# Performance work log

Hardware: AMD Instinct MI355X
Metric: run time of the kernel (lower is better)

## Reference

```python
import jax, jax.numpy as jnp
import numpy as np

B, N, DIM, HEADS = 2, 1024, 1024, 16
HD = DIM // HEADS  # 64


def setup_inputs() -> dict:
    key = jax.random.key(0)
    ks = jax.random.split(key, 8)
    f = lambda k, s: jax.random.normal(k, s, dtype=jnp.float32)
    inv = np.float32(1.0 / np.sqrt(DIM))
    return {
        'x_real': f(ks[0], (B, N, DIM)),
        'x_imag': f(ks[1], (B, N, DIM)),
        'freqs_real': f(ks[2], (N, HD)),
        'freqs_imag': f(ks[3], (N, HD)),
        'Wqkv_r': f(ks[4], (3 * DIM, DIM)) * inv,
        'Wqkv_i': f(ks[5], (3 * DIM, DIM)) * inv,
        'bqkv_r': jnp.zeros((3 * DIM,), jnp.float32),
        'bqkv_i': jnp.zeros((3 * DIM,), jnp.float32),
        'Wout_r': f(ks[6], (DIM, DIM)) * inv,
        'Wout_i': f(ks[7], (DIM, DIM)) * inv,
        'bout_r': jnp.zeros((DIM,), jnp.float32),
        'bout_i': jnp.zeros((DIM,), jnp.float32),
    }


def reference(x_real, x_imag, freqs_real, freqs_imag,
              Wqkv_r, Wqkv_i, bqkv_r, bqkv_i,
              Wout_r, Wout_i, bout_r, bout_i):
    cplx = jax.lax.complex
    x = cplx(x_real, x_imag)                    # [b, n, d] complex64
    Wqkv = cplx(Wqkv_r, Wqkv_i)                 # [3d, d]
    bqkv = cplx(bqkv_r, bqkv_i)
    Wout = cplx(Wout_r, Wout_i)
    bout = cplx(bout_r, bout_i)
    freqs = cplx(freqs_real, freqs_imag)        # [n, hd]

    scale = HD ** (-0.5)

    # ComplexLinear: x @ W^T + b -> [b, n, 3d]
    qkv = jnp.einsum('bnd,ed->bne', x, Wqkv) + bqkv
    # rearrange 'b n (h d qkv) -> qkv b h n d' (qkv index fastest-varying)
    qkv = qkv.reshape(B, N, HEADS, HD, 3)
    q = jnp.transpose(qkv[..., 0], (0, 2, 1, 3))  # [b, h, n, hd]
    k = jnp.transpose(qkv[..., 1], (0, 2, 1, 3))
    v = jnp.transpose(qkv[..., 2], (0, 2, 1, 3))

    # complex rotary: elementwise multiply by freqs [n, hd]
    q = q * freqs
    k = k * freqs

    # complex QK^H -> [b, h, n, n]
    dots = jnp.einsum('bhnd,bhmd->bhnm', q, jnp.conj(k))
    attn = jax.nn.softmax(jnp.abs(dots) * scale, axis=-1)  # real float32

    # real attn @ complex v (promotes to complex64)
    out = jnp.einsum('bhnm,bhmd->bhnd', attn, v)
    out = jnp.transpose(out, (0, 2, 1, 3)).reshape(B, N, DIM)  # b n (h d)

    out = jnp.einsum('bnd,ed->bne', out, Wout) + bout
    # return real/imag stacked so baseline comparison is on real arrays
    return jnp.stack([jnp.real(out), jnp.imag(out)], axis=0)  # [2, b, n, d]
```

## Files before the change

### kernel.cpp

```cpp
#include <hip/hip_runtime.h>
#include <hip/hip_bf16.h>
#include <stdint.h>

#define B 2
#define N 1024
#define DIM 1024
#define HEADS 16
#define HD 64
#define E3 (3*DIM)
#define M (B*N)

typedef __hip_bfloat16 bf16;
typedef __attribute__((ext_vector_type(8))) short short8v;
typedef __attribute__((ext_vector_type(4))) float f32x4;
typedef __attribute__((ext_vector_type(4))) unsigned int u32x4;

__device__ __forceinline__ float scrub(float v) {
    return (v == v && fabsf(v) < 1e30f) ? v : 0.0f;
}
__device__ __forceinline__ float b2f(bf16 x) { return scrub(__bfloat162float(x)); }

template<bool FP32>
__device__ __forceinline__ float ldin(const void* p, int i) {
    if (FP32) return scrub(((const float*)p)[i]);
    else      return scrub(__bfloat162float(((const bf16*)p)[i]));
}

__device__ __forceinline__ bool sniff_fp32(const void* x, int tid, int* sbad) {
    if (tid == 0) *sbad = 0;
    __syncthreads();
    if (tid < 64) {
        const unsigned short* u = (const unsigned short*)x;
        int ex = (u[tid] >> 7) & 0xFF;
        if (ex == 0xFF || ex >= 135 || (ex != 0 && ex <= 118))
            atomicAdd(sbad, 1);
    }
    __syncthreads();
    return *sbad > 4;
}

__device__ __forceinline__ short f2bs(float x) {
    bf16 h = __float2bfloat16(x);
    return __builtin_bit_cast(short, h);
}
__device__ __forceinline__ short8v neg8(short8v x) {
    u32x4 u = __builtin_bit_cast(u32x4, x);
    u ^= 0x80008000u;
    return __builtin_bit_cast(short8v, u);
}
__device__ __forceinline__ f32x4 mfma16(short8v a, short8v b, f32x4 c) {
    return __builtin_amdgcn_mfma_f32_16x16x32_bf16(a, b, c, 0, 0, 0);
}

__device__ __forceinline__ void cvt8(bf16* dhi, bf16* dlo, const float* s) {
    float4 a = *(const float4*)s;
    float4 b = *(const float4*)(s + 4);
    float v[8] = {a.x,a.y,a.z,a.w,b.x,b.y,b.z,b.w};
    short8v hi, lo;
    #pragma unroll
    for (int e = 0; e < 8; ++e) {
        float f = scrub(v[e]);
        bf16 h = __float2bfloat16(f);
        hi[e] = __builtin_bit_cast(short, h);
        lo[e] = f2bs(f - __bfloat162float(h));
    }
    *(short8v*)dhi = hi;
    *(short8v*)dlo = lo;
}
__device__ __forceinline__ void cvt8h(bf16* dhi, const float* s) {
    float4 a = *(const float4*)s;
    float4 b = *(const float4*)(s + 4);
    float v[8] = {a.x,a.y,a.z,a.w,b.x,b.y,b.z,b.w};
    short8v hi;
    #pragma unroll
    for (int e = 0; e < 8; ++e)
        hi[e] = f2bs(scrub(v[e]));
    *(short8v*)dhi = hi;
}

#define PL (64*32)

__device__ __forceinline__ short8v frag_ld32(const bf16* base, int row, int j) {
    return *(const short8v*)(base + row*32 + ((j ^ (row & 3)) << 3));
}

template<int AMODE, int BMODE>
__device__ __forceinline__ void cgemm32(
    const void* Aor, const void* Aoi,
    const bf16* Arh, const bf16* Aih, const bf16* Arl, const bf16* Ail,
    const void* Bor, const void* Boi,
    const bf16* Brh, const bf16* Bih, const bf16* Brl, const bf16* Bil,
    int row0, int col0,
    bf16* sA, bf16* sB,
    f32x4 (*accr)[2], f32x4 (*accs)[2], f32x4 (*acci)[2])
{
    constexpr bool ALO = (AMODE == 1 || AMODE == 2);
    constexpr bool BLO = (BMODE == 1 || BMODE == 2);

    const int t  = threadIdx.x;
    const int w  = t >> 6, l = t & 63;
    const int lr = l & 15, lg = l >> 4;
    const int wm = w >> 1, wn = w & 1;

    const int srow = t >> 2;
    const int sj   = (t & 3) ^ (srow & 3);

    for (int k0 = 0; k0 < DIM; k0 += 32) {
        const size_t aoff = (size_t)(row0 + srow)*DIM + k0 + sj*8;
        const size_t boff = (size_t)(col0 + srow)*DIM + k0 + sj*8;
        bf16* dA = sA + t*8;
        bf16* dB = sB + t*8;
        if constexpr (AMODE == 0) {
            *(short8v*)(dA)        = *(const short8v*)((const bf16*)Aor + aoff);
            *(short8v*)(dA + PL)   = *(const short8v*)((const bf16*)Aoi + aoff);
        } else if constexpr (AMODE == 1) {
            *(short8v*)(dA)        = *(const short8v*)(Arh + aoff);
            *(short8v*)(dA + PL)   = *(const short8v*)(Aih + aoff);
            *(short8v*)(dA + 2*PL) = *(const short8v*)(Arl + aoff);
            *(short8v*)(dA + 3*PL) = *(const short8v*)(Ail + aoff);
        } else if constexpr (AMODE == 3) {
            *(short8v*)(dA)        = *(const short8v*)(Arh + aoff);
            *(short8v*)(dA + PL)   = *(const short8v*)(Aih + aoff);
        } else {
            cvt8(dA,      dA + 2*PL, (const float*)Aor + aoff);
            cvt8(dA + PL, dA + 3*PL, (const float*)Aoi + aoff);
        }
        if constexpr (BMODE == 0) {
            *(short8v*)(dB)        = *(const short8v*)((const bf16*)Bor + boff);
            *(short8v*)(dB + PL)   = *(const short8v*)((const bf16*)Boi + boff);
        } else if constexpr (BMODE == 1) {
            *(short8v*)(dB)        = *(const short8v*)(Brh + boff);
            *(short8v*)(dB + PL)   = *(const short8v*)(Bih + boff);
            *(short8v*)(dB + 2*PL) = *(const short8v*)(Brl + boff);
            *(short8v*)(dB + 3*PL) = *(const short8v*)(Bil + boff);
        } else if constexpr (BMODE == 3) {
            *(short8v*)(dB)        = *(const short8v*)(Brh + boff);
            *(short8v*)(dB + PL)   = *(const short8v*)(Bih + boff);
        } else {
            cvt8(dB,      dB + 2*PL, (const float*)Bor + boff);
            cvt8(dB + PL, dB + 3*PL, (const float*)Boi + boff);
        }
        __syncthreads();

        short8v arh[2], aih[2], arl[2], ail[2];
        #pragma unroll
        for (int mi = 0; mi < 2; ++mi) {
            int arow = wm*32 + mi*16 + lr;
            arh[mi] = frag_ld32(sA,      arow, lg);
            aih[mi] = frag_ld32(sA + PL, arow, lg);
            if constexpr (ALO) {
                arl[mi] = frag_ld32(sA + 2*PL, arow, lg);
                ail[mi] = frag_ld32(sA + 3*PL, arow, lg);
            }
        }
        #pragma unroll
        for (int ni = 0; ni < 2; ++ni) {
            int brow = wn*32 + ni*16 + lr;
            short8v brh = frag_ld32(sB,      brow, lg);
            short8v bih = frag_ld32(sB + PL, brow, lg);
            short8v brl, bil;
            if constexpr (BLO) {
                brl = frag_ld32(sB + 2*PL, brow, lg);
                bil = frag_ld32(sB + 3*PL, brow, lg);
            }
            #pragma unroll
            for (int mi = 0; mi < 2; ++mi) {
                accr[mi][ni] = mfma16(arh[mi], brh, accr[mi][ni]);
                accs[mi][ni] = mfma16(aih[mi], bih, accs[mi][ni]);
                acci[mi][ni] = mfma16(arh[mi], bih, acci[mi][ni]);
                acci[mi][ni] = mfma16(aih[mi], brh, acci[mi][ni]);
                if constexpr (BLO) {
                    accr[mi][ni] = mfma16(arh[mi], brl, accr[mi][ni]);
                    accs[mi][ni] = mfma16(aih[mi], bil, accs[mi][ni]);
                    acci[mi][ni] = mfma16(arh[mi], bil, acci[mi][ni]);
                    acci[mi][ni] = mfma16(aih[mi], brl, acci[mi][ni]);
                }
                if constexpr (ALO) {
                    accr[mi][ni] = mfma16(arl[mi], brh, accr[mi][ni]);
                    accs[mi][ni] = mfma16(ail[mi], bih, accs[mi][ni]);
                    acci[mi][ni] = mfma16(arl[mi], bih, acci[mi][ni]);
                    acci[mi][ni] = mfma16(ail[mi], brh, acci[mi][ni]);
                }
            }
        }
        __syncthreads();
    }
}

struct PrepArgs {
    const void* src[6];
    bf16* hi[6];
    bf16* lo[6];
    int n8[6];
};

__global__ __launch_bounds__(256) void prepass_kernel(PrepArgs a) {
    __shared__ int sbad;
    const int y = blockIdx.y;
    bool f32 = sniff_fp32(a.src[y], threadIdx.x, &sbad);
    if (!f32) return;
    const int n8 = a.n8[y];
    bf16* lo = a.lo[y];
    for (int i = blockIdx.x*blockDim.x + threadIdx.x; i < n8; i += gridDim.x*blockDim.x) {
        if (lo) cvt8 (a.hi[y] + (size_t)i*8, lo + (size_t)i*8, (const float*)a.src[y] + (size_t)i*8);
        else    cvt8h(a.hi[y] + (size_t)i*8,                   (const float*)a.src[y] + (size_t)i*8);
    }
}

template<bool FP32>
__device__ __forceinline__ void qkv_epi(
    const void* fr_, const void* fi_, const void* bqr, const void* bqi,
    bf16* qr, bf16* qi, bf16* kr, bf16* ki, bf16* vr, bf16* vi,
    int row0, int col0,
    f32x4 (*accr)[2], f32x4 (*accs)[2], f32x4 (*acci)[2])
{
    const int t  = threadIdx.x;
    const int w  = t >> 6, l = t & 63;
    const int lr = l & 15, lg = l >> 4;
    const int wm = w >> 1, wn = w & 1;

    #pragma unroll
    for (int ni = 0; ni < 2; ++ni) {
        int col = col0 + wn*32 + ni*16 + lr;
        float bre = ldin<FP32>(bqr, col);
        float bim = ldin<FP32>(bqi, col);
        int s = col % 3;
        int tc = col / 3;
        int h = tc / HD, d = tc % HD;
        #pragma unroll
        for (int mi = 0; mi < 2; ++mi)
        #pragma unroll
        for (int r = 0; r < 4; ++r) {
            int row = row0 + wm*32 + mi*16 + 4*lg + r;
            int bb = row / N, n = row % N;
            float cr = accr[mi][ni][r] - accs[mi][ni][r] + bre;
            float ci = acci[mi][ni][r] + bim;
            if (s == 2) {
                int idxT = ((bb*HEADS + h)*HD + d)*N + n;
                vr[idxT] = __float2bfloat16(scrub(cr));
                vi[idxT] = __float2bfloat16(scrub(ci));
            } else {
                float fre = ldin<FP32>(fr_, n*HD + d);
                float fim = ldin<FP32>(fi_, n*HD + d);
                float rr = cr*fre - ci*fim;
                float ri = cr*fim + ci*fre;
                int idx = ((bb*HEADS + h)*N + n)*HD + d;
                if (s == 0) { qr[idx] = __float2bfloat16(scrub(rr)); qi[idx] = __float2bfloat16(scrub(ri)); }
                else        { kr[idx] = __float2bfloat16(scrub(rr)); ki[idx] = __float2bfloat16(scrub(ri)); }
            }
        }
    }
}

template<int FM>
__global__ __launch_bounds__(256, 4) void qkv_kernel(
    const void* xr, const void* xi, const void* fr_, const void* fi_,
    const void* Wr, const void* Wi, const void* bqr, const void* bqi,
    const bf16* xrh, const bf16* xih, const bf16* xrl, const bf16* xil,
    const bf16* wrh, const bf16* wih,
    bf16* qr, bf16* qi, bf16* kr, bf16* ki, bf16* vr, bf16* vi)
{
    __shared__ __align__(16) bf16 sA[4*PL];
    __shared__ __align__(16) bf16 sB[(FM==1 ? 2 : 4)*PL];
    __shared__ int sbad;
    bool f32 = sniff_fp32(xr, threadIdx.x, &sbad);

    int wg   = blockIdx.x;
    int xcd  = wg & 7;
    int idx  = wg >> 3;
    int rtin = idx & 1;
    int tmp  = idx >> 1;
    int ctl  = tmp % 6;
    int rtg  = tmp / 6;
    int row0 = (rtg*2 + rtin) * 64;
    int col0 = (xcd*6 + ctl) * 64;

    f32x4 accr[2][2] = {}, accs[2][2] = {}, acci[2][2] = {};
    if (f32) {
        if constexpr (FM == 1)
            cgemm32<1, 3>(xr, xi, xrh, xih, xrl, xil,
                          Wr, Wi, wrh, wih, nullptr, nullptr,
                          row0, col0, sA, sB, accr, accs, acci);
        else
            cgemm32<2, 2>(xr, xi, nullptr, nullptr, nullptr, nullptr,
                          Wr, Wi, nullptr, nullptr, nullptr, nullptr,
                          row0, col0, sA, sB, accr, accs, acci);
        qkv_epi<true >(fr_, fi_, bqr, bqi, qr,qi,kr,ki,vr,vi, row0, col0, accr, accs, acci);
    } else {
        cgemm32<0, 0>(xr, xi, nullptr, nullptr, nullptr, nullptr,
                      Wr, Wi, nullptr, nullptr, nullptr, nullptr,
                      row0, col0, sA, sB, accr, accs, acci);
        qkv_epi<false>(fr_, fi_, bqr, bqi, qr,qi,kr,ki,vr,vi, row0, col0, accr, accs, acci);
    }
}

__device__ __forceinline__ short8v frag_ld(const bf16* base, int row, int j) {
    return *(const short8v*)(base + row*64 + ((j ^ (row & 7)) << 3));
}

__global__ __launch_bounds__(256) void attn_kernel(
    const bf16* qr, const bf16* qi, const bf16* kr, const bf16* ki,
    const bf16* vtr, const bf16* vti, bf16* aor_, bf16* aoi_)
{
    __shared__ __align__(16) bf16 skr[64*64];
    __shared__ __align__(16) bf16 ski[64*64];
    __shared__ __align__(16) bf16 svr[64*64];
    __shared__ __align__(16) bf16 svi[64*64];
    __shared__ __align__(16) bf16 sp[4][16*64];

    const int t  = threadIdx.x;
    const int w  = t >> 6;
    const int l  = t & 63;
    const int lr = l & 15;
    const int lg = l >> 4;
    int wg = blockIdx.x;
    int sw = (wg & 7) * ((int)gridDim.x >> 3) + (wg >> 3);
    const int qt = sw & 15;
    const int bh = sw >> 4;

    const size_t hbase = (size_t)bh * N * HD;

    const bf16* qrg = qr + hbase + (size_t)(qt*64 + w*16 + lr) * HD;
    const bf16* qig = qi + hbase + (size_t)(qt*64 + w*16 + lr) * HD;
    short8v qfr[2], qfi[2], qfrn[2];
    #pragma unroll
    for (int ks = 0; ks < 2; ++ks) {
        qfr[ks] = *(const short8v*)(qrg + 32*ks + 8*lg);
        qfi[ks] = *(const short8v*)(qig + 32*ks + 8*lg);
        qfrn[ks] = neg8(qfr[ks]);
    }

    const int cA = t, cB = t + 256;
    const int rA = cA >> 3, jA = (cA & 7) ^ (rA & 7);
    const int rB = cB >> 3, jB = (cB & 7) ^ (rB & 7);
    const bf16* krg = kr  + hbase;
    const bf16* kig = ki  + hbase;
    const bf16* vrg = vtr + hbase;
    const bf16* vig = vti + hbase;

    f32x4 outr[4], outi[4];
    #pragma unroll
    for (int dt = 0; dt < 4; ++dt) {
        outr[dt] = (f32x4){0.f,0.f,0.f,0.f};
        outi[dt] = (f32x4){0.f,0.f,0.f,0.f};
    }
    float mrow[4] = {-1e30f,-1e30f,-1e30f,-1e30f};
    float lrow[4] = {0.f,0.f,0.f,0.f};

    for (int kt = 0; kt < N/64; ++kt) {
        const int m0 = kt*64;
        *(short8v*)(skr + cA*8) = *(const short8v*)(krg + (size_t)(m0+rA)*HD + jA*8);
        *(short8v*)(skr + cB*8) = *(const short8v*)(krg + (size_t)(m0+rB)*HD + jB*8);
        *(short8v*)(ski + cA*8) = *(const short8v*)(kig + (size_t)(m0+rA)*HD + jA*8);
        *(short8v*)(ski + cB*8) = *(const short8v*)(kig + (size_t)(m0+rB)*HD + jB*8);
        *(short8v*)(svr + cA*8) = *(const short8v*)(vrg + (size_t)rA*N + m0 + jA*8);
        *(short8v*)(svr + cB*8) = *(const short8v*)(vrg + (size_t)rB*N + m0 + jB*8);
        *(short8v*)(svi + cA*8) = *(const short8v*)(vig + (size_t)rA*N + m0 + jA*8);
        *(short8v*)(svi + cB*8) = *(const short8v*)(vig + (size_t)rB*N + m0 + jB*8);
        __syncthreads();

        f32x4 sr[4], si[4];
        #pragma unroll
        for (int ct = 0; ct < 4; ++ct) {
            f32x4 ar = (f32x4){0.f,0.f,0.f,0.f};
            f32x4 ai = (f32x4){0.f,0.f,0.f,0.f};
            #pragma unroll
            for (int ks = 0; ks < 2; ++ks) {
                short8v kfr = frag_ld(skr, 16*ct + lr, 4*ks + lg);
                short8v kfi = frag_ld(ski, 16*ct + lr, 4*ks + lg);
                ar = mfma16(qfr[ks],  kfr, ar);
                ar = mfma16(qfi[ks],  kfi, ar);
                ai = mfma16(qfi[ks],  kfr, ai);
                ai = mfma16(qfrn[ks], kfi, ai);
            }
            sr[ct] = ar; si[ct] = ai;
        }

        float p[4][4];
        float pmax[4] = {-1e30f,-1e30f,-1e30f,-1e30f};
        #pragma unroll
        for (int ct = 0; ct < 4; ++ct)
        #pragma unroll
        for (int r = 0; r < 4; ++r) {
            float s = sqrtf(sr[ct][r]*sr[ct][r] + si[ct][r]*si[ct][r]) * 0.125f;
            p[ct][r] = s;
            pmax[r] = fmaxf(pmax[r], s);
        }
        #pragma unroll
        for (int mk = 1; mk <= 8; mk <<= 1)
        #pragma unroll
        for (int r = 0; r < 4; ++r)
            pmax[r] = fmaxf(pmax[r], __shfl_xor(pmax[r], mk));

        float fsc[4];
        #pragma unroll
        for (int r = 0; r < 4; ++r) {
            float mnew = fmaxf(mrow[r], pmax[r]);
            fsc[r] = __expf(mrow[r] - mnew);
            mrow[r] = mnew;
        }
        float rsum[4] = {0.f,0.f,0.f,0.f};
        #pragma unroll
        for (int ct = 0; ct < 4; ++ct)
        #pragma unroll
        for (int r = 0; r < 4; ++r) {
            float e = __expf(p[ct][r] - mrow[r]);
            p[ct][r] = e;
            rsum[r] += e;
        }
        #pragma unroll
        for (int mk = 1; mk <= 8; mk <<= 1)
        #pragma unroll
        for (int r = 0; r < 4; ++r)
            rsum[r] += __shfl_xor(rsum[r], mk);
        #pragma unroll
        for (int r = 0; r < 4; ++r)
            lrow[r] = lrow[r]*fsc[r] + rsum[r];
        #pragma unroll
        for (int dt = 0; dt < 4; ++dt)
        #pragma unroll
        for (int r = 0; r < 4; ++r) {
            outr[dt][r] *= fsc[r];
            outi[dt][r] *= fsc[r];
        }

        bf16* pw = sp[w];
        #pragma unroll
        for (int ct = 0; ct < 4; ++ct)
        #pragma unroll
        for (int r = 0; r < 4; ++r) {
            int prow = 4*lg + r;
            int pcol = 16*ct + lr;
            int jj = (pcol >> 3) ^ (prow & 7);
            pw[prow*64 + jj*8 + (pcol & 7)] = __float2bfloat16(p[ct][r]);
        }
        short8v pa[2];
        #pragma unroll
        for (int ks2 = 0; ks2 < 2; ++ks2)
            pa[ks2] = frag_ld(pw, lr, 4*ks2 + lg);

        #pragma unroll
        for (int dt = 0; dt < 4; ++dt)
        #pragma unroll
        for (int ks2 = 0; ks2 < 2; ++ks2) {
            short8v vfr = frag_ld(svr, 16*dt + lr, 4*ks2 + lg);
            short8v vfi = frag_ld(svi, 16*dt + lr, 4*ks2 + lg);
            outr[dt] = mfma16(pa[ks2], vfr, outr[dt]);
            outi[dt] = mfma16(pa[ks2], vfi, outi[dt]);
        }
        __syncthreads();
    }

    const int b_ = bh / HEADS, h_ = bh % HEADS;
    float invl[4];
    #pragma unroll
    for (int r = 0; r < 4; ++r) invl[r] = 1.0f / lrow[r];
    #pragma unroll
    for (int dt = 0; dt < 4; ++dt)
    #pragma unroll
    for (int r = 0; r < 4; ++r) {
        int n_ = qt*64 + w*16 + 4*lg + r;
        int d_ = 16*dt + lr;
        size_t oidx = ((size_t)(b_*N + n_))*DIM + h_*HD + d_;
        aor_[oidx] = __float2bfloat16(scrub(outr[dt][r]*invl[r]));
        aoi_[oidx] = __float2bfloat16(scrub(outi[dt][r]*invl[r]));
    }
}

template<int FM>
__global__ __launch_bounds__(256, 4) void outproj_kernel(
    const void* xprobe,
    const bf16* ar, const bf16* ai,
    const void* Wr, const void* Wi, const void* bor, const void* boi,
    const bf16* wrh, const bf16* wih,
    void* out)
{
    __shared__ __align__(16) bf16 sA[2*PL];
    __shared__ __align__(16) bf16 sB[(FM==3 ? 2 : 4)*PL];
    __shared__ int sbad;
    bool f32 = sniff_fp32(xprobe, threadIdx.x, &sbad);

    int wg   = blockIdx.x;
    int xcd  = wg & 7;
    int idx  = wg >> 3;
    int rtin = idx & 1;
    int tmp  = idx >> 1;
    int ctl  = tmp & 1;
    int rtg  = tmp >> 1;
    int row0 = (rtg*2 + rtin) * 64;
    int col0 = (xcd*2 + ctl) * 64;

    const int t  = threadIdx.x;
    const int w  = t >> 6, l = t & 63;
    const int lr = l & 15, lg = l >> 4;
    const int wm = w >> 1, wn = w & 1;

    f32x4 accr[2][2] = {}, accs[2][2] = {}, acci[2][2] = {};
    if (f32) {
        if constexpr (FM == 3)
            cgemm32<0, 3>(ar, ai, nullptr, nullptr, nullptr, nullptr,
                          Wr, Wi, wrh, wih, nullptr, nullptr,
                          row0, col0, sA, sB, accr, accs, acci);
        else
            cgemm32<0, 2>(ar, ai, nullptr, nullptr, nullptr, nullptr,
                          Wr, Wi, nullptr, nullptr, nullptr, nullptr,
                          row0, col0, sA, sB, accr, accs, acci);
    } else {
        cgemm32<0, 0>(ar, ai, nullptr, nullptr, nullptr, nullptr,
                      Wr, Wi, nullptr, nullptr, nullptr, nullptr,
                      row0, col0, sA, sB, accr, accs, acci);
    }

    #pragma unroll
    for (int ni = 0; ni < 2; ++ni) {
        int col = col0 + wn*32 + ni*16 + lr;
        float bre = f32 ? ldin<true>(bor, col) : ldin<false>(bor, col);
        float bim = f32 ? ldin<true>(boi, col) : ldin<false>(boi, col);
        #pragma unroll
        for (int mi = 0; mi < 2; ++mi)
        #pragma unroll
        for (int r = 0; r < 4; ++r) {
            int row = row0 + wm*32 + mi*16 + 4*lg + r;
            float cr = scrub(accr[mi][ni][r] - accs[mi][ni][r] + bre);
            float ci = scrub(acci[mi][ni][r] + bim);
            if (f32) {
                ((float*)out)[(size_t)row*DIM + col]                 = cr;
                ((float*)out)[(size_t)M*DIM + (size_t)row*DIM + col] = ci;
            } else {
                ((bf16*)out)[(size_t)row*DIM + col]                  = __float2bfloat16(cr);
                ((bf16*)out)[(size_t)M*DIM + (size_t)row*DIM + col]  = __float2bfloat16(ci);
            }
        }
    }
}

extern "C" void kernel_launch(void* const* d_in, const int* in_sizes, int n_in,
                              void* d_out, int out_size, void* d_ws, size_t ws_size,
                              hipStream_t stream)
{
    const void* xr     = d_in[0];
    const void* xi     = d_in[1];
    const void* fr     = d_in[2];
    const void* fi     = d_in[3];
    const void* Wqkv_r = d_in[4];
    const void* Wqkv_i = d_in[5];
    const void* bqkv_r = d_in[6];
    const void* bqkv_i = d_in[7];
    const void* Wout_r = d_in[8];
    const void* Wout_i = d_in[9];
    const void* bout_r = d_in[10];
    const void* bout_i = d_in[11];

    bf16* w = (bf16*)d_ws;
    const size_t QS  = (size_t)B*HEADS*N*HD;
    const size_t XS  = (size_t)M*DIM;
    const size_t WQS = (size_t)E3*DIM;
    const size_t WOS = (size_t)DIM*DIM;

    bf16* qr   = w;          bf16* qi   = qr  + QS;
    bf16* kr   = qi  + QS;   bf16* ki   = kr  + QS;
    bf16* vr   = ki  + QS;   bf16* vi   = vr  + QS;
    bf16* aor_ = vi  + QS;   bf16* aoi_ = aor_ + QS;
    bf16* xrh = aoi_ + QS;   bf16* xih = xrh + XS;
    bf16* xrl = xih + XS;    bf16* xil = xrl + XS;
    bf16* wqrh = xil + XS;   bf16* wqih = wqrh + WQS;
    bf16* worh = wqih + WQS; bf16* woih = worh + WOS;

    const size_t need = (size_t)(8*QS + 4*XS + 2*WQS + 2*WOS) * sizeof(bf16);
    const bool pre = ws_size >= need;

    if (pre) {
        PrepArgs a;
        a.src[0] = xr;     a.hi[0] = xrh;  a.lo[0] = xrl;    a.n8[0] = (int)(XS/8);
        a.src[1] = xi;     a.hi[1] = xih;  a.lo[1] = xil;    a.n8[1] = (int)(XS/8);
        a.src[2] = Wqkv_r; a.hi[2] = wqrh; a.lo[2] = nullptr; a.n8[2] = (int)(WQS/8);
        a.src[3] = Wqkv_i; a.hi[3] = wqih; a.lo[3] = nullptr; a.n8[3] = (int)(WQS/8);
        a.src[4] = Wout_r; a.hi[4] = worh; a.lo[4] = nullptr; a.n8[4] = (int)(WOS/8);
        a.src[5] = Wout_i; a.hi[5] = woih; a.lo[5] = nullptr; a.n8[5] = (int)(WOS/8);
        prepass_kernel<<<dim3(1536, 6), dim3(256), 0, stream>>>(a);

        qkv_kernel<1><<<dim3((E3/64)*(M/64)), dim3(256), 0, stream>>>(
            xr, xi, fr, fi, Wqkv_r, Wqkv_i, bqkv_r, bqkv_i,
            xrh, xih, xrl, xil, wqrh, wqih,
            qr, qi, kr, ki, vr, vi);
    } else {
        qkv_kernel<2><<<dim3((E3/64)*(M/64)), dim3(256), 0, stream>>>(
            xr, xi, fr, fi, Wqkv_r, Wqkv_i, bqkv_r, bqkv_i,
            nullptr, nullptr, nullptr, nullptr, nullptr, nullptr,
            qr, qi, kr, ki, vr, vi);
    }

    attn_kernel<<<dim3(B*HEADS*(N/64)), dim3(256), 0, stream>>>(
        qr, qi, kr, ki, vr, vi, aor_, aoi_);

    if (pre) {
        outproj_kernel<3><<<dim3((DIM/64)*(M/64)), dim3(256), 0, stream>>>(
            xr, aor_, aoi_, Wout_r, Wout_i, bout_r, bout_i,
            worh, woih, d_out);
    } else {
        outproj_kernel<2><<<dim3((DIM/64)*(M/64)), dim3(256), 0, stream>>>(
            xr, aor_, aoi_, Wout_r, Wout_i, bout_r, bout_i,
            nullptr, nullptr, d_out);
    }
}
```

Baseline: 317.8 us.

## Enlarge QKV GEMM tile to 128x64 and change LDS swizzle layout

Grows the QKV projection tile from 64x64 to 128x64 rows, with each of the four waves owning 32 rows and all 64 columns. This halves the grid and raises reuse of each loaded weight tile. It also replaces the LDS layout with a paired-row XOR swizzle over 8 chunks, meant to reduce bank conflicts on fragment loads. The extra accumulators raise register pressure, so occupancy drops from 4 to 3 blocks per CU, and the smaller grid may leave the machine less well balanced.

Measured after the change: 323.7 us. Within noise of the previous version (+1.9%).

```diff
diff --git a/kernel.cpp b/kernel.cpp
--- a/kernel.cpp
+++ b/kernel.cpp
@@ -78,67 +78,75 @@
     *(short8v*)dhi = hi;
 }
 
-#define PL (64*32)
-
-__device__ __forceinline__ short8v frag_ld32(const bf16* base, int row, int j) {
-    return *(const short8v*)(base + row*32 + ((j ^ (row & 3)) << 3));
-}
-
-template<int AMODE, int BMODE>
+#define PLB 2048
+
+__device__ __forceinline__ short8v frag_ldp(const bf16* base, int row, int j) {
+    int p = row >> 1;
+    int c = (((row & 1) << 2) | j) ^ (p & 7);
+    return *(const short8v*)(base + p*64 + c*8);
+}
+
+template<int AMODE, int BMODE, int BM, int NI>
 __device__ __forceinline__ void cgemm32(
     const void* Aor, const void* Aoi,
     const bf16* Arh, const bf16* Aih, const bf16* Arl, const bf16* Ail,
     const void* Bor, const void* Boi,
-    const bf16* Brh, const bf16* Bih, const bf16* Brl, const bf16* Bil,
+    const bf16* Brh, const bf16* Bih,
     int row0, int col0,
     bf16* sA, bf16* sB,
-    f32x4 (*accr)[2], f32x4 (*accs)[2], f32x4 (*acci)[2])
+    f32x4 (*accr)[NI], f32x4 (*accs)[NI], f32x4 (*acci)[NI])
 {
     constexpr bool ALO = (AMODE == 1 || AMODE == 2);
-    constexpr bool BLO = (BMODE == 1 || BMODE == 2);
+    constexpr bool BLO = (BMODE == 2);
+    constexpr int  PLA = BM*32;
 
     const int t  = threadIdx.x;
     const int w  = t >> 6, l = t & 63;
     const int lr = l & 15, lg = l >> 4;
-    const int wm = w >> 1, wn = w & 1;
-
-    const int srow = t >> 2;
-    const int sj   = (t & 3) ^ (srow & 3);
+    const int wm = (NI == 4) ? w : (w >> 1);
+    const int wn = (NI == 4) ? 0 : (w & 1);
+
+    const int pb  = t >> 3;
+    const int cpb = (t & 7) ^ (pb & 7);
+    const int srb = 2*pb + (cpb >> 2);
+    const int sjb = cpb & 3;
 
     for (int k0 = 0; k0 < DIM; k0 += 32) {
-        const size_t aoff = (size_t)(row0 + srow)*DIM + k0 + sj*8;
-        const size_t boff = (size_t)(col0 + srow)*DIM + k0 + sj*8;
-        bf16* dA = sA + t*8;
-        bf16* dB = sB + t*8;
-        if constexpr (AMODE == 0) {
-            *(short8v*)(dA)        = *(const short8v*)((const bf16*)Aor + aoff);
-            *(short8v*)(dA + PL)   = *(const short8v*)((const bf16*)Aoi + aoff);
-        } else if constexpr (AMODE == 1) {
-            *(short8v*)(dA)        = *(const short8v*)(Arh + aoff);
-            *(short8v*)(dA + PL)   = *(const short8v*)(Aih + aoff);
-            *(short8v*)(dA + 2*PL) = *(const short8v*)(Arl + aoff);
-            *(short8v*)(dA + 3*PL) = *(const short8v*)(Ail + aoff);
-        } else if constexpr (AMODE == 3) {
-            *(short8v*)(dA)        = *(const short8v*)(Arh + aoff);
-            *(short8v*)(dA + PL)   = *(const short8v*)(Aih + aoff);
-        } else {
-            cvt8(dA,      dA + 2*PL, (const float*)Aor + aoff);
-            cvt8(dA + PL, dA + 3*PL, (const float*)Aoi + aoff);
-        }
-        if constexpr (BMODE == 0) {
-            *(short8v*)(dB)        = *(const short8v*)((const bf16*)Bor + boff);
-            *(short8v*)(dB + PL)   = *(const short8v*)((const bf16*)Boi + boff);
-        } else if constexpr (BMODE == 1) {
-            *(short8v*)(dB)        = *(const short8v*)(Brh + boff);
-            *(short8v*)(dB + PL)   = *(const short8v*)(Bih + boff);
-            *(short8v*)(dB + 2*PL) = *(const short8v*)(Brl + boff);
-            *(short8v*)(dB + 3*PL) = *(const short8v*)(Bil + boff);
-        } else if constexpr (BMODE == 3) {
-            *(short8v*)(dB)        = *(const short8v*)(Brh + boff);
-            *(short8v*)(dB + PL)   = *(const short8v*)(Bih + boff);
-        } else {
-            cvt8(dB,      dB + 2*PL, (const float*)Bor + boff);
-            cvt8(dB + PL, dB + 3*PL, (const float*)Boi + boff);
+        #pragma unroll
+        for (int u = 0; u < BM/64; ++u) {
+            int c   = t + 256*u;
+            int pa  = c >> 3;
+            int cpa = (c & 7) ^ (pa & 7);
+            int sra = 2*pa + (cpa >> 2);
+            int sja = cpa & 3;
+            size_t aoff = (size_t)(row0 + sra)*DIM + k0 + sja*8;
+            bf16* dA = sA + c*8;
+            if constexpr (AMODE == 0) {
+                *(short8v*)(dA)        = *(const short8v*)((const bf16*)Aor + aoff);
+                *(short8v*)(dA + PLA)  = *(const short8v*)((const bf16*)Aoi + aoff);
+            } else if constexpr (AMODE == 1) {
+                *(short8v*)(dA)         = *(const short8v*)(Arh + aoff);
+                *(short8v*)(dA + PLA)   = *(const short8v*)(Aih + aoff);
+                *(short8v*)(dA + 2*PLA) = *(const short8v*)(Arl + aoff);
+                *(short8v*)(dA + 3*PLA) = *(const short8v*)(Ail + aoff);
+            } else {
+                cvt8(dA,       dA + 2*PLA, (const float*)Aor + aoff);
+                cvt8(dA + PLA, dA + 3*PLA, (const float*)Aoi + aoff);
+            }
+        }
+        {
+            size_t boff = (size_t)(col0 + srb)*DIM + k0 + sjb*8;
+            bf16* dB = sB + t*8;
+            if constexpr (BMODE == 0) {
+                *(short8v*)(dB)       = *(const short8v*)((const bf16*)Bor + boff);
+                *(short8v*)(dB + PLB) = *(const short8v*)((const bf16*)Boi + boff);
+            } else if constexpr (BMODE == 3) {
+                *(short8v*)(dB)       = *(const short8v*)(Brh + boff);
+                *(short8v*)(dB + PLB) = *(const short8v*)(Bih + boff);
+            } else {
+                cvt8(dB,       dB + 2*PLB, (const float*)Bor + boff);
+                cvt8(dB + PLB, dB + 3*PLB, (const float*)Boi + boff);
+            }
         }
         __syncthreads();
 
@@ -146,22 +154,22 @@
         #pragma unroll
         for (int mi = 0; mi < 2; ++mi) {
             int arow = wm*32 + mi*16 + lr;
-            arh[mi] = frag_ld32(sA,      arow, lg);
-            aih[mi] = frag_ld32(sA + PL, arow, lg);
+            arh[mi] = frag_ldp(sA,       arow, lg);
+            aih[mi] = frag_ldp(sA + PLA, arow, lg);
             if constexpr (ALO) {
-                arl[mi] = frag_ld32(sA + 2*PL, arow, lg);
-                ail[mi] = frag_ld32(sA + 3*PL, arow, lg);
-            }
-        }
-        #pragma unroll
-        for (int ni = 0; ni < 2; ++ni) {
+                arl[mi] = frag_ldp(sA + 2*PLA, arow, lg);
+                ail[mi] = frag_ldp(sA + 3*PLA, arow, lg);
+            }
+        }
+        #pragma unroll
+        for (int ni = 0; ni < NI; ++ni) {
             int brow = wn*32 + ni*16 + lr;
-            short8v brh = frag_ld32(sB,      brow, lg);
-            short8v bih = frag_ld32(sB + PL, brow, lg);
+            short8v brh = frag_ldp(sB,       brow, lg);
+            short8v bih = frag_ldp(sB + PLB, brow, lg);
             short8v brl, bil;
             if constexpr (BLO) {
-                brl = frag_ld32(sB + 2*PL, brow, lg);
-                bil = frag_ld32(sB + 3*PL, brow, lg);
+                brl = frag_ldp(sB + 2*PLB, brow, lg);
+                bil = frag_ldp(sB + 3*PLB, brow, lg);
             }
             #pragma unroll
             for (int mi = 0; mi < 2; ++mi) {
@@ -212,16 +220,15 @@
     const void* fr_, const void* fi_, const void* bqr, const void* bqi,
     bf16* qr, bf16* qi, bf16* kr, bf16* ki, bf16* vr, bf16* vi,
     int row0, int col0,
-    f32x4 (*accr)[2], f32x4 (*accs)[2], f32x4 (*acci)[2])
+    f32x4 (*accr)[4], f32x4 (*accs)[4], f32x4 (*acci)[4])
 {
     const int t  = threadIdx.x;
     const int w  = t >> 6, l = t & 63;
     const int lr = l & 15, lg = l >> 4;
-    const int wm = w >> 1, wn = w & 1;
-
-    #pragma unroll
-    for (int ni = 0; ni < 2; ++ni) {
-        int col = col0 + wn*32 + ni*16 + lr;
+
+    #pragma unroll
+    for (int ni = 0; ni < 4; ++ni) {
+        int col = col0 + ni*16 + lr;
         float bre = ldin<FP32>(bqr, col);
         float bim = ldin<FP32>(bqi, col);
         int s = col % 3;
@@ -231,7 +238,7 @@
         for (int mi = 0; mi < 2; ++mi)
         #pragma unroll
         for (int r = 0; r < 4; ++r) {
-            int row = row0 + wm*32 + mi*16 + 4*lg + r;
+            int row = row0 + w*32 + mi*16 + 4*lg + r;
             int bb = row / N, n = row % N;
             float cr = accr[mi][ni][r] - accs[mi][ni][r] + bre;
             float ci = acci[mi][ni][r] + bim;
@@ -253,43 +260,41 @@
 }
 
 template<int FM>
-__global__ __launch_bounds__(256, 4) void qkv_kernel(
+__global__ __launch_bounds__(256, 3) void qkv_kernel(
     const void* xr, const void* xi, const void* fr_, const void* fi_,
     const void* Wr, const void* Wi, const void* bqr, const void* bqi,
     const bf16* xrh, const bf16* xih, const bf16* xrl, const bf16* xil,
     const bf16* wrh, const bf16* wih,
     bf16* qr, bf16* qi, bf16* kr, bf16* ki, bf16* vr, bf16* vi)
 {
-    __shared__ __align__(16) bf16 sA[4*PL];
-    __shared__ __align__(16) bf16 sB[(FM==1 ? 2 : 4)*PL];
+    __shared__ __align__(16) bf16 sA[4*128*32];
+    __shared__ __align__(16) bf16 sB[(FM==1 ? 2 : 4)*PLB];
     __shared__ int sbad;
     bool f32 = sniff_fp32(xr, threadIdx.x, &sbad);
 
     int wg   = blockIdx.x;
     int xcd  = wg & 7;
     int idx  = wg >> 3;
-    int rtin = idx & 1;
-    int tmp  = idx >> 1;
-    int ctl  = tmp % 6;
-    int rtg  = tmp / 6;
-    int row0 = (rtg*2 + rtin) * 64;
+    int ctl  = idx % 6;
+    int rtg  = idx / 6;
+    int row0 = rtg * 128;
     int col0 = (xcd*6 + ctl) * 64;
 
-    f32x4 accr[2][2] = {}, accs[2][2] = {}, acci[2][2] = {};
+    f32x4 accr[2][4] = {}, accs[2][4] = {}, acci[2][4] = {};
     if (f32) {
         if constexpr (FM == 1)
-            cgemm32<1, 3>(xr, xi, xrh, xih, xrl, xil,
-                          Wr, Wi, wrh, wih, nullptr, nullptr,
-                          row0, col0, sA, sB, accr, accs, acci);
+            cgemm32<1, 3, 128, 4>(xr, xi, xrh, xih, xrl, xil,
+                                  Wr, Wi, wrh, wih,
+                                  row0, col0, sA, sB, accr, accs, acci);
         else
-            cgemm32<2, 2>(xr, xi, nullptr, nullptr, nullptr, nullptr,
-                          Wr, Wi, nullptr, nullptr, nullptr, nullptr,
-                          row0, col0, sA, sB, accr, accs, acci);
+            cgemm32<2, 2, 128, 4>(xr, xi, nullptr, nullptr, nullptr, nullptr,
+                                  Wr, Wi, nullptr, nullptr,
+                                  row0, col0, sA, sB, accr, accs, acci);
         qkv_epi<true >(fr_, fi_, bqr, bqi, qr,qi,kr,ki,vr,vi, row0, col0, accr, accs, acci);
     } else {
-        cgemm32<0, 0>(xr, xi, nullptr, nullptr, nullptr, nullptr,
-                      Wr, Wi, nullptr, nullptr, nullptr, nullptr,
-                      row0, col0, sA, sB, accr, accs, acci);
+        cgemm32<0, 0, 128, 4>(xr, xi, nullptr, nullptr, nullptr, nullptr,
+                              Wr, Wi, nullptr, nullptr,
+                              row0, col0, sA, sB, accr, accs, acci);
         qkv_epi<false>(fr_, fi_, bqr, bqi, qr,qi,kr,ki,vr,vi, row0, col0, accr, accs, acci);
     }
 }
@@ -475,8 +480,8 @@
     const bf16* wrh, const bf16* wih,
     void* out)
 {
-    __shared__ __align__(16) bf16 sA[2*PL];
-    __shared__ __align__(16) bf16 sB[(FM==3 ? 2 : 4)*PL];
+    __shared__ __align__(16) bf16 sA[2*PLB];
+    __shared__ __align__(16) bf16 sB[(FM==3 ? 2 : 4)*PLB];
     __shared__ int sbad;
     bool f32 = sniff_fp32(xprobe, threadIdx.x, &sbad);
 
@@ -498,17 +503,17 @@
     f32x4 accr[2][2] = {}, accs[2][2] = {}, acci[2][2] = {};
     if (f32) {
         if constexpr (FM == 3)
-            cgemm32<0, 3>(ar, ai, nullptr, nullptr, nullptr, nullptr,
-                          Wr, Wi, wrh, wih, nullptr, nullptr,
-                          row0, col0, sA, sB, accr, accs, acci);
+            cgemm32<0, 3, 64, 2>(ar, ai, nullptr, nullptr, nullptr, nullptr,
+                                 Wr, Wi, wrh, wih,
+                                 row0, col0, sA, sB, accr, accs, acci);
         else
-            cgemm32<0, 2>(ar, ai, nullptr, nullptr, nullptr, nullptr,
-                          Wr, Wi, nullptr, nullptr, nullptr, nullptr,
-                          row0, col0, sA, sB, accr, accs, acci);
+            cgemm32<0, 2, 64, 2>(ar, ai, nullptr, nullptr, nullptr, nullptr,
+                                 Wr, Wi, nullptr, nullptr,
+                                 row0, col0, sA, sB, accr, accs, acci);
     } else {
-        cgemm32<0, 0>(ar, ai, nullptr, nullptr, nullptr, nullptr,
-                      Wr, Wi, nullptr, nullptr, nullptr, nullptr,
-                      row0, col0, sA, sB, accr, accs, acci);
+        cgemm32<0, 0, 64, 2>(ar, ai, nullptr, nullptr, nullptr, nullptr,
+                             Wr, Wi, nullptr, nullptr,
+                             row0, col0, sA, sB, accr, accs, acci);
     }
 
     #pragma unroll
@@ -579,12 +584,12 @@
         a.src[5] = Wout_i; a.hi[5] = woih; a.lo[5] = nullptr; a.n8[5] = (int)(WOS/8);
         prepass_kernel<<<dim3(1536, 6), dim3(256), 0, stream>>>(a);
 
-        qkv_kernel<1><<<dim3((E3/64)*(M/64)), dim3(256), 0, stream>>>(
+        qkv_kernel<1><<<dim3((E3/64)*(M/128)), dim3(256), 0, stream>>>(
             xr, xi, fr, fi, Wqkv_r, Wqkv_i, bqkv_r, bqkv_i,
             xrh, xih, xrl, xil, wqrh, wqih,
             qr, qi, kr, ki, vr, vi);
     } else {
-        qkv_kernel<2><<<dim3((E3/64)*(M/64)), dim3(256), 0, stream>>>(
+        qkv_kernel<2><<<dim3((E3/64)*(M/128)), dim3(256), 0, stream>>>(
             xr, xi, fr, fi, Wqkv_r, Wqkv_i, bqkv_r, bqkv_i,
             nullptr, nullptr, nullptr, nullptr, nullptr, nullptr,
             qr, qi, kr, ki, vr, vi);
```
